# Performance work log

Hardware: AMD Instinct MI355X
Metric: run time of the kernel (lower is better)

## Reference

```python
import jax, jax.numpy as jnp
import numpy as np

N = 1_500_000
CB, CT, CO, B = 96, 128, 96, 8
BN_EPS = 1e-5


def setup_inputs() -> dict:
    key = jax.random.key(0)
    k1, k2, k3, k4 = jax.random.split(key, 4)
    return {
        "backbone_F": jax.random.normal(k1, (N, CB), dtype=jnp.float32),
        "batch_idx": jax.random.randint(k2, (N,), 0, B, dtype=jnp.int32),
        "text_feats": jax.random.normal(k3, (B, CT), dtype=jnp.float32),
        "W": jax.random.normal(k4, (CB + CT, CO), dtype=jnp.float32) * (1.0 / np.sqrt(CB + CT)),
        "gamma": jnp.ones((CO,), dtype=jnp.float32),
        "beta": jnp.zeros((CO,), dtype=jnp.float32),
    }


def reference(backbone_F, batch_idx, text_feats, W, gamma, beta):
    # gather text feats per point via batch index: [N, CT]
    rep_text = text_feats[batch_idx]
    # concat backbone + text feats: [N, CB+CT]
    combined = jnp.concatenate([backbone_F, rep_text], axis=1)
    # 1x1 sparse conv == pointwise GEMM (no bias): [N, CO]
    x = combined @ W
    # BatchNorm (training mode: batch stats over the N points)
    mean = jnp.mean(x, axis=0)
    var = jnp.var(x, axis=0)
    x = (x - mean) * jax.lax.rsqrt(var + BN_EPS) * gamma + beta
    # ReLU
    return jnp.maximum(x, 0.0)
```

## Files before the change

kernel.cpp:

```cpp
#include <hip/hip_runtime.h>
#include <hip/hip_bf16.h>

#define N_PTS 1500000
#define NT_TILES (N_PTS / 16)
#define CBCH 96
#define CTCH 128
#define COCH 96
#define NB 8
#define BN_EPS 1e-5f
#define GRID1 512
#define STPAD 100

#define GSUM_OFF 0
#define GSQ_OFF 96
#define T_OFF 384

typedef __attribute__((ext_vector_type(8))) short bf16x8;
typedef __attribute__((ext_vector_type(4))) float f32x4;

__device__ __forceinline__ short f2bf(float f) {
    __hip_bfloat16 h = __float2bfloat16(f);
    short s;
    __builtin_memcpy(&s, &h, sizeof(s));
    return s;
}

__global__ void k0_init(const float* __restrict__ text, const float* __restrict__ W,
                        float* __restrict__ ws) {
    if (blockIdx.x == NB) {
        for (int i = threadIdx.x; i < 192; i += blockDim.x) ws[i] = 0.f;
        return;
    }
    int b = blockIdx.x;
    int c = threadIdx.x;
    if (c < COCH) {
        float acc = 0.f;
        #pragma unroll 8
        for (int k = 0; k < CTCH; ++k)
            acc += text[b * CTCH + k] * W[(CBCH + k) * COCH + c];
        ws[T_OFF + b * COCH + c] = acc;
    }
}


__device__ __forceinline__ void stage_W(const float* __restrict__ W, short* sW) {
    for (int i = threadIdx.x; i < CBCH * COCH; i += blockDim.x) {
        int k = i / COCH, c = i % COCH;
        int ct = c >> 4, lr = c & 15;
        int kt = k >> 5, grp = (k >> 3) & 3, j = k & 7;
        sW[(((ct * 3 + kt) * 64) + (grp * 16 + lr)) * 8 + j] = f2bf(W[i]);
    }
}

__device__ __forceinline__ void load_bfrag_lds(const short* sW, int lane, bf16x8 bf[6][3]) {
    #pragma unroll
    for (int ct = 0; ct < 6; ++ct)
        #pragma unroll
        for (int kt = 0; kt < 3; ++kt)
            bf[ct][kt] = *reinterpret_cast<const bf16x8*>(sW + ((ct * 3 + kt) * 64 + lane) * 8);
}

__device__ __forceinline__ void tile_acc(const float* __restrict__ bb,
                                         const int* __restrict__ bidx,
                                         const float* __restrict__ sT,
                                         const bf16x8 bf[6][3],
                                         int base, int grp, int lr,
                                         f32x4 acc[6]) {
    int b = bidx[base + lr];
    #pragma unroll
    for (int ct = 0; ct < 6; ++ct)
        acc[ct] = *reinterpret_cast<const f32x4*>(&sT[b * STPAD + ct * 16 + grp * 4]);

    bf16x8 pf[3];
    #pragma unroll
    for (int kt = 0; kt < 3; ++kt) {
        const f32x4* p = reinterpret_cast<const f32x4*>(bb + (size_t)(base + lr) * CBCH + kt * 32 + grp * 8);
        f32x4 x0 = p[0], x1 = p[1];
        #pragma unroll
        for (int j = 0; j < 4; ++j) {
            pf[kt][j]     = f2bf(x0[j]);
            pf[kt][4 + j] = f2bf(x1[j]);
        }
    }
    #pragma unroll
    for (int ct = 0; ct < 6; ++ct)
        #pragma unroll
        for (int kt = 0; kt < 3; ++kt)
            acc[ct] = __builtin_amdgcn_mfma_f32_16x16x32_bf16(bf[ct][kt], pf[kt], acc[ct], 0, 0, 0);
}

__global__ __launch_bounds__(256, 2) void k1_stats(const float* __restrict__ bb,
                                                   const int* __restrict__ bidx,
                                                   const float* __restrict__ W,
                                                   float* __restrict__ ws) {
    __shared__ __align__(16) short sW[6 * 3 * 64 * 8];
    __shared__ __align__(16) float sT[NB * STPAD];
    __shared__ float sredS[4][COCH];
    __shared__ float sredQ[4][COCH];

    stage_W(W, sW);
    for (int i = threadIdx.x; i < NB * COCH; i += blockDim.x)
        sT[(i / COCH) * STPAD + (i % COCH)] = ws[T_OFF + i];
    __syncthreads();

    const int lane = threadIdx.x & 63;
    const int wv = threadIdx.x >> 6;
    const int grp = lane >> 4, lr = lane & 15;

    bf16x8 bf[6][3];
    load_bfrag_lds(sW, lane, bf);

    f32x4 sum[6], sq[6];
    #pragma unroll
    for (int ct = 0; ct < 6; ++ct) { sum[ct] = (f32x4)0.f; sq[ct] = (f32x4)0.f; }

    const int gw = blockIdx.x * 4 + wv;
    for (int t = gw; t < NT_TILES; t += GRID1 * 4) {
        int base = t * 16;
        f32x4 acc[6];
        tile_acc(bb, bidx, sT, bf, base, grp, lr, acc);
        #pragma unroll
        for (int ct = 0; ct < 6; ++ct) {
            sum[ct] += acc[ct];
            sq[ct] += acc[ct] * acc[ct];
        }
    }

    #pragma unroll
    for (int ct = 0; ct < 6; ++ct)
        #pragma unroll
        for (int r = 0; r < 4; ++r) {
            float s = sum[ct][r], q = sq[ct][r];
            s += __shfl_xor(s, 1);  q += __shfl_xor(q, 1);
            s += __shfl_xor(s, 2);  q += __shfl_xor(q, 2);
            s += __shfl_xor(s, 4);  q += __shfl_xor(q, 4);
            s += __shfl_xor(s, 8);  q += __shfl_xor(q, 8);
            if (lr == 0) {
                sredS[wv][ct * 16 + grp * 4 + r] = s;
                sredQ[wv][ct * 16 + grp * 4 + r] = q;
            }
        }
    __syncthreads();
    if (threadIdx.x < COCH) {
        int c = threadIdx.x;
        atomicAdd(&ws[GSUM_OFF + c], sredS[0][c] + sredS[1][c] + sredS[2][c] + sredS[3][c]);
        atomicAdd(&ws[GSQ_OFF + c],  sredQ[0][c] + sredQ[1][c] + sredQ[2][c] + sredQ[3][c]);
    }
}

__global__ __launch_bounds__(256, 2) void k3_out(const float* __restrict__ bb,
                                                 const int* __restrict__ bidx,
                                                 const float* __restrict__ W,
                                                 const float* __restrict__ gamma,
                                                 const float* __restrict__ beta,
                                                 const float* __restrict__ ws,
                                                 float* __restrict__ out) {
    __shared__ __align__(16) short sW[6 * 3 * 64 * 8];
    __shared__ __align__(16) float sT[NB * STPAD];
    __shared__ __align__(16) float sScale[COCH];
    __shared__ __align__(16) float sBias[COCH];

    stage_W(W, sW);
    for (int i = threadIdx.x; i < NB * COCH; i += blockDim.x)
        sT[(i / COCH) * STPAD + (i % COCH)] = ws[T_OFF + i];
    if (threadIdx.x < COCH) {
        int c = threadIdx.x;
        float mean = ws[GSUM_OFF + c] * (1.f / (float)N_PTS);
        float var  = ws[GSQ_OFF + c] * (1.f / (float)N_PTS) - mean * mean;
        float scl  = gamma[c] * rsqrtf(var + BN_EPS);
        sScale[c] = scl;
        sBias[c]  = beta[c] - mean * scl;
    }
    __syncthreads();

    const int lane = threadIdx.x & 63;
    const int wv = threadIdx.x >> 6;
    const int grp = lane >> 4, lr = lane & 15;

    bf16x8 bf[6][3];
    load_bfrag_lds(sW, lane, bf);

    f32x4 sc[6], bs[6];
    #pragma unroll
    for (int ct = 0; ct < 6; ++ct) {
        sc[ct] = *reinterpret_cast<const f32x4*>(&sScale[ct * 16 + grp * 4]);
        bs[ct] = *reinterpret_cast<const f32x4*>(&sBias[ct * 16 + grp * 4]);
    }

    const int gw = blockIdx.x * 4 + wv;
    for (int t = NT_TILES - 1 - gw; t >= 0; t -= GRID1 * 4) {
        int base = t * 16;
        f32x4 acc[6];
        tile_acc(bb, bidx, sT, bf, base, grp, lr, acc);
        #pragma unroll
        for (int ct = 0; ct < 6; ++ct) {
            f32x4 y;
            #pragma unroll
            for (int r = 0; r < 4; ++r)
                y[r] = fmaxf(acc[ct][r] * sc[ct][r] + bs[ct][r], 0.f);
            __builtin_nontemporal_store(y,
                reinterpret_cast<f32x4*>(out + (size_t)(base + lr) * COCH + ct * 16 + grp * 4));
        }
    }
}

extern "C" void kernel_launch(void* const* d_in, const int* in_sizes, int n_in,
                              void* d_out, int out_size, void* d_ws, size_t ws_size,
                              hipStream_t stream) {
    const float* bb    = (const float*)d_in[0];
    const int*   bidx  = (const int*)d_in[1];
    const float* text  = (const float*)d_in[2];
    const float* W     = (const float*)d_in[3];
    const float* gamma = (const float*)d_in[4];
    const float* beta  = (const float*)d_in[5];
    float* out = (float*)d_out;
    float* ws  = (float*)d_ws;

    hipLaunchKernelGGL(k0_init, dim3(NB + 1), dim3(128), 0, stream, text, W, ws);
    hipLaunchKernelGGL(k1_stats, dim3(GRID1), dim3(256), 0, stream, bb, bidx, W, ws);
    hipLaunchKernelGGL(k3_out, dim3(GRID1), dim3(256), 0, stream, bb, bidx, W, gamma, beta, ws, out);
}
```

Baseline: 369.3 us.

## Stash bf16 GEMM results in stats pass and normalize from stash

The stats kernel now writes the pre-normalization GEMM outputs as bf16 into the workspace when it is large enough. A lightweight elementwise kernel then applies BN scale/bias and ReLU from that stash instead of re-reading the backbone features and redoing the GEMM. Backbone loads in the stats pass become nontemporal. Total memory traffic is about the same, since stash write plus read replaces the second backbone read. Rounding outputs to bf16 also adds precision loss.

```diff
diff --git a/kernel.cpp b/kernel.cpp
--- a/kernel.cpp
+++ b/kernel.cpp
@@ -9,13 +9,18 @@
 #define NB 8
 #define BN_EPS 1e-5f
 #define GRID1 512
+#define NWAVE (GRID1 * 4)
 #define STPAD 100
 
 #define GSUM_OFF 0
 #define GSQ_OFF 96
 #define T_OFF 384
+#define STASH_OFF_F 1024
+#define STASH_BYTES ((size_t)N_PTS * COCH * 2)
+#define WS_NEEDED (STASH_OFF_F * 4 + STASH_BYTES)
 
 typedef __attribute__((ext_vector_type(8))) short bf16x8;
+typedef __attribute__((ext_vector_type(8))) short short8;
 typedef __attribute__((ext_vector_type(4))) float f32x4;
 
 __device__ __forceinline__ short f2bf(float f) {
@@ -60,6 +65,7 @@
             bf[ct][kt] = *reinterpret_cast<const bf16x8*>(sW + ((ct * 3 + kt) * 64 + lane) * 8);
 }
 
+template <bool NTLOAD>
 __device__ __forceinline__ void tile_acc(const float* __restrict__ bb,
                                          const int* __restrict__ bidx,
                                          const float* __restrict__ sT,
@@ -75,7 +81,9 @@
     #pragma unroll
     for (int kt = 0; kt < 3; ++kt) {
         const f32x4* p = reinterpret_cast<const f32x4*>(bb + (size_t)(base + lr) * CBCH + kt * 32 + grp * 8);
-        f32x4 x0 = p[0], x1 = p[1];
+        f32x4 x0, x1;
+        if (NTLOAD) { x0 = __builtin_nontemporal_load(p); x1 = __builtin_nontemporal_load(p + 1); }
+        else        { x0 = p[0]; x1 = p[1]; }
         #pragma unroll
         for (int j = 0; j < 4; ++j) {
             pf[kt][j]     = f2bf(x0[j]);
@@ -92,7 +100,8 @@
 __global__ __launch_bounds__(256, 2) void k1_stats(const float* __restrict__ bb,
                                                    const int* __restrict__ bidx,
                                                    const float* __restrict__ W,
-                                                   float* __restrict__ ws) {
+                                                   float* __restrict__ ws,
+                                                   int do_stash) {
     __shared__ __align__(16) short sW[6 * 3 * 64 * 8];
     __shared__ __align__(16) float sT[NB * STPAD];
     __shared__ float sredS[4][COCH];
@@ -110,19 +119,30 @@
     bf16x8 bf[6][3];
     load_bfrag_lds(sW, lane, bf);
 
+    short* stash = (short*)(ws + STASH_OFF_F);
+
     f32x4 sum[6], sq[6];
     #pragma unroll
     for (int ct = 0; ct < 6; ++ct) { sum[ct] = (f32x4)0.f; sq[ct] = (f32x4)0.f; }
 
     const int gw = blockIdx.x * 4 + wv;
-    for (int t = gw; t < NT_TILES; t += GRID1 * 4) {
+    for (int t = gw; t < NT_TILES; t += NWAVE) {
         int base = t * 16;
         f32x4 acc[6];
-        tile_acc(bb, bidx, sT, bf, base, grp, lr, acc);
+        tile_acc<true>(bb, bidx, sT, bf, base, grp, lr, acc);
         #pragma unroll
         for (int ct = 0; ct < 6; ++ct) {
             sum[ct] += acc[ct];
             sq[ct] += acc[ct] * acc[ct];
+        }
+        if (do_stash) {
+            #pragma unroll
+            for (int ct = 0; ct < 6; ++ct) {
+                unsigned lo = (unsigned short)f2bf(acc[ct][0]) | ((unsigned)(unsigned short)f2bf(acc[ct][1]) << 16);
+                unsigned hi = (unsigned short)f2bf(acc[ct][2]) | ((unsigned)(unsigned short)f2bf(acc[ct][3]) << 16);
+                uint2 v = {lo, hi};
+                *reinterpret_cast<uint2*>(stash + (size_t)(base + lr) * COCH + ct * 16 + grp * 4) = v;
+            }
         }
     }
 
@@ -148,13 +168,56 @@
     }
 }
 
-__global__ __launch_bounds__(256, 2) void k3_out(const float* __restrict__ bb,
-                                                 const int* __restrict__ bidx,
-                                                 const float* __restrict__ W,
-                                                 const float* __restrict__ gamma,
-                                                 const float* __restrict__ beta,
-                                                 const float* __restrict__ ws,
-                                                 float* __restrict__ out) {
+__global__ __launch_bounds__(256, 8) void k2s(const float* __restrict__ gamma,
+                                              const float* __restrict__ beta,
+                                              const float* __restrict__ ws,
+                                              float* __restrict__ out) {
+    __shared__ __align__(16) float sScale[COCH];
+    __shared__ __align__(16) float sBias[COCH];
+    if (threadIdx.x < COCH) {
+        int c = threadIdx.x;
+        float mean = ws[GSUM_OFF + c] * (1.f / (float)N_PTS);
+        float var  = ws[GSQ_OFF + c] * (1.f / (float)N_PTS) - mean * mean;
+        float scl  = gamma[c] * rsqrtf(var + BN_EPS);
+        sScale[c] = scl;
+        sBias[c]  = beta[c] - mean * scl;
+    }
+    __syncthreads();
+
+    const short8* stash8 = (const short8*)(ws + STASH_OFF_F);
+    const long U = (long)N_PTS * COCH / 8;
+    const long stride = (long)gridDim.x * blockDim.x;
+    const long gtid = (long)blockIdx.x * blockDim.x + threadIdx.x;
+
+    for (long u = U - 1 - gtid; u >= 0; u -= stride) {
+        unsigned c12 = (unsigned)(u % 12u);
+        int cb = (int)c12 * 8;
+        short8 s = stash8[u];
+        f32x4 sc0 = *reinterpret_cast<const f32x4*>(&sScale[cb]);
+        f32x4 sc1 = *reinterpret_cast<const f32x4*>(&sScale[cb + 4]);
+        f32x4 bs0 = *reinterpret_cast<const f32x4*>(&sBias[cb]);
+        f32x4 bs1 = *reinterpret_cast<const f32x4*>(&sBias[cb + 4]);
+        f32x4 y0, y1;
+        #pragma unroll
+        for (int j = 0; j < 4; ++j) {
+            float x0 = __uint_as_float(((unsigned)(unsigned short)s[j]) << 16);
+            float x1 = __uint_as_float(((unsigned)(unsigned short)s[4 + j]) << 16);
+            y0[j] = fmaxf(x0 * sc0[j] + bs0[j], 0.f);
+            y1[j] = fmaxf(x1 * sc1[j] + bs1[j], 0.f);
+        }
+        f32x4* o = reinterpret_cast<f32x4*>(out + u * 8);
+        __builtin_nontemporal_store(y0, o);
+        __builtin_nontemporal_store(y1, o + 1);
+    }
+}
+
+__global__ __launch_bounds__(256, 2) void k3_fb(const float* __restrict__ bb,
+                                                const int* __restrict__ bidx,
+                                                const float* __restrict__ W,
+                                                const float* __restrict__ gamma,
+                                                const float* __restrict__ beta,
+                                                const float* __restrict__ ws,
+                                                float* __restrict__ out) {
     __shared__ __align__(16) short sW[6 * 3 * 64 * 8];
     __shared__ __align__(16) float sT[NB * STPAD];
     __shared__ __align__(16) float sScale[COCH];
@@ -188,10 +251,10 @@
     }
 
     const int gw = blockIdx.x * 4 + wv;
-    for (int t = NT_TILES - 1 - gw; t >= 0; t -= GRID1 * 4) {
+    for (int t = NT_TILES - 1 - gw; t >= 0; t -= NWAVE) {
         int base = t * 16;
         f32x4 acc[6];
-        tile_acc(bb, bidx, sT, bf, base, grp, lr, acc);
+        tile_acc<false>(bb, bidx, sT, bf, base, grp, lr, acc);
         #pragma unroll
         for (int ct = 0; ct < 6; ++ct) {
             f32x4 y;
@@ -216,7 +279,13 @@
     float* out = (float*)d_out;
     float* ws  = (float*)d_ws;
 
+    const int do_stash = (ws_size >= WS_NEEDED) ? 1 : 0;
+
     hipLaunchKernelGGL(k0_init, dim3(NB + 1), dim3(128), 0, stream, text, W, ws);
-    hipLaunchKernelGGL(k1_stats, dim3(GRID1), dim3(256), 0, stream, bb, bidx, W, ws);
-    hipLaunchKernelGGL(k3_out, dim3(GRID1), dim3(256), 0, stream, bb, bidx, W, gamma, beta, ws, out);
-}
+    hipLaunchKernelGGL(k1_stats, dim3(GRID1), dim3(256), 0, stream, bb, bidx, W, ws, do_stash);
+    if (do_stash) {
+        hipLaunchKernelGGL(k2s, dim3(2048), dim3(256), 0, stream, gamma, beta, ws, out);
+    } else {
+        hipLaunchKernelGGL(k3_fb, dim3(GRID1), dim3(256), 0, stream, bb, bidx, W, gamma, beta, ws, out);
+    }
+}
```

After: 466.2 us. 26.2% more time.

## Compute BN statistics via Gram matrix of inputs instead of full GEMM pass

Applied to the files above, without the earlier changes.

Replaces the stats pass, which ran the full GEMM and reduced the outputs, with a kernel that accumulates the 104x104 Gram matrix of the bf16 backbone features plus one-hot batch columns using MFMA. A single-block solve kernel then derives per-channel sum and sum of squares as W^T G W plus the text-bias terms. This cuts MFMA work and register pressure in the first pass, but it still reads all of backbone_F and adds an LDS transpose, many atomics and an extra serial solve kernel. Stats are computed in a different form, so numerical error may differ slightly.

```diff
diff --git a/kernel.cpp b/kernel.cpp
--- a/kernel.cpp
+++ b/kernel.cpp
@@ -3,17 +3,23 @@
 
 #define N_PTS 1500000
 #define NT_TILES (N_PTS / 16)
+#define NCHUNK (N_PTS / 32)
 #define CBCH 96
 #define CTCH 128
 #define COCH 96
 #define NB 8
 #define BN_EPS 1e-5f
-#define GRID1 512
+#define GRID3 512
+#define NWAVE3 (GRID3 * 4)
+#define GRIDG 1024
 #define STPAD 100
+#define CPAD 36
 
 #define GSUM_OFF 0
 #define GSQ_OFF 96
 #define T_OFF 384
+#define G_OFF 1280
+#define GPITCH 112
 
 typedef __attribute__((ext_vector_type(8))) short bf16x8;
 typedef __attribute__((ext_vector_type(4))) float f32x4;
@@ -24,11 +30,15 @@
     __builtin_memcpy(&s, &h, sizeof(s));
     return s;
 }
+__device__ __forceinline__ float bf2f(short s) {
+    return __uint_as_float(((unsigned)(unsigned short)s) << 16);
+}
 
 __global__ void k0_init(const float* __restrict__ text, const float* __restrict__ W,
                         float* __restrict__ ws) {
     if (blockIdx.x == NB) {
         for (int i = threadIdx.x; i < 192; i += blockDim.x) ws[i] = 0.f;
+        for (int i = threadIdx.x; i < GPITCH * GPITCH; i += blockDim.x) ws[G_OFF + i] = 0.f;
         return;
     }
     int b = blockIdx.x;
@@ -43,6 +53,122 @@
 }
 
 
+__device__ __forceinline__ bf16x8 read_frag(const short* sCh, int tile, int lr, int g) {
+    const short* p = sCh + (tile * 16 + lr) * CPAD + g * 8;
+    union { bf16x8 v; uint2 h[2]; } u;
+    u.h[0] = *reinterpret_cast<const uint2*>(p);
+    u.h[1] = *reinterpret_cast<const uint2*>(p + 4);
+    return u.v;
+}
+
+__global__ __launch_bounds__(256, 2) void k1g(const float* __restrict__ bb,
+                                              const int* __restrict__ bidx,
+                                              float* __restrict__ ws) {
+    __shared__ __align__(16) short sCh[112 * CPAD];
+
+    const int tid = threadIdx.x;
+    const int lane = tid & 63, wv = tid >> 6;
+    const int lr = lane & 15, g = lane >> 4;
+
+    int pi[7], pj[7];
+    {
+        int rem = wv * 7, ii = 0;
+        while (rem >= 7 - ii) { rem -= 7 - ii; ++ii; }
+        int jj = ii + rem;
+        #pragma unroll
+        for (int u = 0; u < 7; ++u) {
+            pi[u] = ii; pj[u] = jj;
+            ++jj; if (jj == 7) { ++ii; jj = ii; }
+        }
+    }
+
+    for (int i = tid; i < 16 * CPAD; i += blockDim.x) sCh[96 * CPAD + i] = 0;
+
+    f32x4 acc[7];
+    #pragma unroll
+    for (int u = 0; u < 7; ++u) acc[u] = (f32x4)0.f;
+
+    for (int ch = blockIdx.x; ch < NCHUNK; ch += GRIDG) {
+        __syncthreads();
+        const float* src = bb + (size_t)ch * 32 * CBCH;
+        #pragma unroll
+        for (int i = 0; i < 3; ++i) {
+            int q = tid + 256 * i;
+            int c = (q * 4) % CBCH, p = (q * 4) / CBCH;
+            f32x4 v = *reinterpret_cast<const f32x4*>(src + q * 4);
+            #pragma unroll
+            for (int j = 0; j < 4; ++j)
+                sCh[(c + j) * CPAD + p] = f2bf(v[j]);
+        }
+        if (tid < 32) {
+            int b = bidx[(size_t)ch * 32 + tid];
+            #pragma unroll
+            for (int bb8 = 0; bb8 < NB; ++bb8)
+                sCh[(96 + bb8) * CPAD + tid] = (bb8 == b) ? (short)0x3F80 : (short)0;
+        }
+        __syncthreads();
+        #pragma unroll
+        for (int u = 0; u < 7; ++u) {
+            bf16x8 fa = read_frag(sCh, pi[u], lr, g);
+            bf16x8 fb = read_frag(sCh, pj[u], lr, g);
+            acc[u] = __builtin_amdgcn_mfma_f32_16x16x32_bf16(fa, fb, acc[u], 0, 0, 0);
+        }
+    }
+
+    #pragma unroll
+    for (int u = 0; u < 7; ++u)
+        #pragma unroll
+        for (int r = 0; r < 4; ++r)
+            atomicAdd(&ws[G_OFF + (pi[u] * 16 + 4 * g + r) * GPITCH + pj[u] * 16 + lr],
+                      acc[u][r]);
+}
+
+__global__ __launch_bounds__(384) void k_solve(const float* __restrict__ W,
+                                               float* __restrict__ ws) {
+    __shared__ short sW16[CBCH * COCH];
+    __shared__ float sQ[4][COCH];
+    const int tid = threadIdx.x;
+    for (int i = tid; i < CBCH * COCH; i += 384) sW16[i] = f2bf(W[i]);
+    __syncthreads();
+
+    const float* Gm = ws + G_OFF;
+    const int c = tid % COCH;
+    const int qq = tid / COCH;
+
+    float accq = 0.f;
+    for (int k = qq * 24; k < qq * 24 + 24; ++k) {
+        float wk = bf2f(sW16[k * COCH + c]);
+        int ti = k >> 4;
+        float inner = 0.f;
+        for (int k2 = 0; k2 < CBCH; ++k2) {
+            int tj = k2 >> 4;
+            int idx = (ti <= tj) ? (k * GPITCH + k2) : (k2 * GPITCH + k);
+            inner += Gm[idx] * bf2f(sW16[k2 * COCH + c]);
+        }
+        accq += wk * inner;
+    }
+    sQ[qq][c] = accq;
+    __syncthreads();
+
+    if (tid < COCH) {
+        float gsq = sQ[0][c] + sQ[1][c] + sQ[2][c] + sQ[3][c];
+        float gsum = 0.f;
+        #pragma unroll
+        for (int b = 0; b < NB; ++b) {
+            float d = 0.f;
+            for (int k = 0; k < CBCH; ++k)
+                d += Gm[k * GPITCH + 96 + b] * bf2f(sW16[k * COCH + c]);
+            float Tc = ws[T_OFF + b * COCH + c];
+            float nb = Gm[(96 + b) * GPITCH + 96 + b];
+            gsum += d + nb * Tc;
+            gsq  += 2.f * Tc * d + nb * Tc * Tc;
+        }
+        ws[GSUM_OFF + c] = gsum;
+        ws[GSQ_OFF + c]  = gsq;
+    }
+}
+
+
 __device__ __forceinline__ void stage_W(const float* __restrict__ W, short* sW) {
     for (int i = threadIdx.x; i < CBCH * COCH; i += blockDim.x) {
         int k = i / COCH, c = i % COCH;
@@ -58,94 +184,6 @@
         #pragma unroll
         for (int kt = 0; kt < 3; ++kt)
             bf[ct][kt] = *reinterpret_cast<const bf16x8*>(sW + ((ct * 3 + kt) * 64 + lane) * 8);
-}
-
-__device__ __forceinline__ void tile_acc(const float* __restrict__ bb,
-                                         const int* __restrict__ bidx,
-                                         const float* __restrict__ sT,
-                                         const bf16x8 bf[6][3],
-                                         int base, int grp, int lr,
-                                         f32x4 acc[6]) {
-    int b = bidx[base + lr];
-    #pragma unroll
-    for (int ct = 0; ct < 6; ++ct)
-        acc[ct] = *reinterpret_cast<const f32x4*>(&sT[b * STPAD + ct * 16 + grp * 4]);
-
-    bf16x8 pf[3];
-    #pragma unroll
-    for (int kt = 0; kt < 3; ++kt) {
-        const f32x4* p = reinterpret_cast<const f32x4*>(bb + (size_t)(base + lr) * CBCH + kt * 32 + grp * 8);
-        f32x4 x0 = p[0], x1 = p[1];
-        #pragma unroll
-        for (int j = 0; j < 4; ++j) {
-            pf[kt][j]     = f2bf(x0[j]);
-            pf[kt][4 + j] = f2bf(x1[j]);
-        }
-    }
-    #pragma unroll
-    for (int ct = 0; ct < 6; ++ct)
-        #pragma unroll
-        for (int kt = 0; kt < 3; ++kt)
-            acc[ct] = __builtin_amdgcn_mfma_f32_16x16x32_bf16(bf[ct][kt], pf[kt], acc[ct], 0, 0, 0);
-}
-
-__global__ __launch_bounds__(256, 2) void k1_stats(const float* __restrict__ bb,
-                                                   const int* __restrict__ bidx,
-                                                   const float* __restrict__ W,
-                                                   float* __restrict__ ws) {
-    __shared__ __align__(16) short sW[6 * 3 * 64 * 8];
-    __shared__ __align__(16) float sT[NB * STPAD];
-    __shared__ float sredS[4][COCH];
-    __shared__ float sredQ[4][COCH];
-
-    stage_W(W, sW);
-    for (int i = threadIdx.x; i < NB * COCH; i += blockDim.x)
-        sT[(i / COCH) * STPAD + (i % COCH)] = ws[T_OFF + i];
-    __syncthreads();
-
-    const int lane = threadIdx.x & 63;
-    const int wv = threadIdx.x >> 6;
-    const int grp = lane >> 4, lr = lane & 15;
-
-    bf16x8 bf[6][3];
-    load_bfrag_lds(sW, lane, bf);
-
-    f32x4 sum[6], sq[6];
-    #pragma unroll
-    for (int ct = 0; ct < 6; ++ct) { sum[ct] = (f32x4)0.f; sq[ct] = (f32x4)0.f; }
-
-    const int gw = blockIdx.x * 4 + wv;
-    for (int t = gw; t < NT_TILES; t += GRID1 * 4) {
-        int base = t * 16;
-        f32x4 acc[6];
-        tile_acc(bb, bidx, sT, bf, base, grp, lr, acc);
-        #pragma unroll
-        for (int ct = 0; ct < 6; ++ct) {
-            sum[ct] += acc[ct];
-            sq[ct] += acc[ct] * acc[ct];
-        }
-    }
-
-    #pragma unroll
-    for (int ct = 0; ct < 6; ++ct)
-        #pragma unroll
-        for (int r = 0; r < 4; ++r) {
-            float s = sum[ct][r], q = sq[ct][r];
-            s += __shfl_xor(s, 1);  q += __shfl_xor(q, 1);
-            s += __shfl_xor(s, 2);  q += __shfl_xor(q, 2);
-            s += __shfl_xor(s, 4);  q += __shfl_xor(q, 4);
-            s += __shfl_xor(s, 8);  q += __shfl_xor(q, 8);
-            if (lr == 0) {
-                sredS[wv][ct * 16 + grp * 4 + r] = s;
-                sredQ[wv][ct * 16 + grp * 4 + r] = q;
-            }
-        }
-    __syncthreads();
-    if (threadIdx.x < COCH) {
-        int c = threadIdx.x;
-        atomicAdd(&ws[GSUM_OFF + c], sredS[0][c] + sredS[1][c] + sredS[2][c] + sredS[3][c]);
-        atomicAdd(&ws[GSQ_OFF + c],  sredQ[0][c] + sredQ[1][c] + sredQ[2][c] + sredQ[3][c]);
-    }
 }
 
 __global__ __launch_bounds__(256, 2) void k3_out(const float* __restrict__ bb,
@@ -188,10 +226,31 @@
     }
 
     const int gw = blockIdx.x * 4 + wv;
-    for (int t = NT_TILES - 1 - gw; t >= 0; t -= GRID1 * 4) {
+    for (int t = NT_TILES - 1 - gw; t >= 0; t -= NWAVE3) {
         int base = t * 16;
+        int b = bidx[base + lr];
         f32x4 acc[6];
-        tile_acc(bb, bidx, sT, bf, base, grp, lr, acc);
+        #pragma unroll
+        for (int ct = 0; ct < 6; ++ct)
+            acc[ct] = *reinterpret_cast<const f32x4*>(&sT[b * STPAD + ct * 16 + grp * 4]);
+
+        bf16x8 pf[3];
+        #pragma unroll
+        for (int kt = 0; kt < 3; ++kt) {
+            const f32x4* p = reinterpret_cast<const f32x4*>(bb + (size_t)(base + lr) * CBCH + kt * 32 + grp * 8);
+            f32x4 x0 = p[0], x1 = p[1];
+            #pragma unroll
+            for (int j = 0; j < 4; ++j) {
+                pf[kt][j]     = f2bf(x0[j]);
+                pf[kt][4 + j] = f2bf(x1[j]);
+            }
+        }
+        #pragma unroll
+        for (int ct = 0; ct < 6; ++ct)
+            #pragma unroll
+            for (int kt = 0; kt < 3; ++kt)
+                acc[ct] = __builtin_amdgcn_mfma_f32_16x16x32_bf16(bf[ct][kt], pf[kt], acc[ct], 0, 0, 0);
+
         #pragma unroll
         for (int ct = 0; ct < 6; ++ct) {
             f32x4 y;
@@ -217,6 +276,7 @@
     float* ws  = (float*)d_ws;
 
     hipLaunchKernelGGL(k0_init, dim3(NB + 1), dim3(128), 0, stream, text, W, ws);
-    hipLaunchKernelGGL(k1_stats, dim3(GRID1), dim3(256), 0, stream, bb, bidx, W, ws);
-    hipLaunchKernelGGL(k3_out, dim3(GRID1), dim3(256), 0, stream, bb, bidx, W, gamma, beta, ws, out);
-}
+    hipLaunchKernelGGL(k1g, dim3(GRIDG), dim3(256), 0, stream, bb, bidx, ws);
+    hipLaunchKernelGGL(k_solve, dim3(1), dim3(384), 0, stream, W, ws);
+    hipLaunchKernelGGL(k3_out, dim3(GRID3), dim3(256), 0, stream, bb, bidx, W, gamma, beta, ws, out);
+}
```

New measurement: 519.0 us. 1.41x slower.
